# Kernel tuning notes

Hardware: AMD Instinct MI355X
Metric: run time of the kernel (lower is better)

## Reference

```python
import jax, jax.numpy as jnp
import numpy as np

D_MODEL = 1024
NHEAD = 16
HEAD_DIM = D_MODEL // NHEAD  # 64
THETA = 10000.0


def apply_rope(t):
    # t: [B, H, S, D]. Interleaved-pair RoPE (lucidrains rotary-embedding-torch
    # rotate_queries_or_keys), positions = arange(S), theta = 10000.
    B, H, S, D = t.shape
    inv_freq = 1.0 / (THETA ** (jnp.arange(0, D, 2, dtype=jnp.float32) / D))  # [D/2]
    ang = jnp.arange(S, dtype=jnp.float32)[:, None] * inv_freq               # [S, D/2]
    cos = jnp.cos(ang).astype(t.dtype)
    sin = jnp.sin(ang).astype(t.dtype)
    tp = t.reshape(B, H, S, D // 2, 2)
    x1, x2 = tp[..., 0], tp[..., 1]
    rot = jnp.stack([x1 * cos - x2 * sin, x1 * sin + x2 * cos], axis=-1)
    return rot.reshape(B, H, S, D)


def setup_inputs() -> dict:
    key = jax.random.key(0)
    k0, k1, k2, k3, k4 = jax.random.split(key, 5)
    B, Sx, Sc = 2, 2048, 2048
    sc = 0.02  # weight init scale
    return {
        "x": jax.random.normal(k0, (B, Sx, D_MODEL), jnp.float32),
        "context": jax.random.normal(k1, (B, Sc, D_MODEL), jnp.float32),
        "Wq": jax.random.normal(k2, (D_MODEL, D_MODEL), jnp.float32) * sc,
        "Wv": jax.random.normal(k3, (D_MODEL, D_MODEL), jnp.float32) * sc,
        "Wo": jax.random.normal(k4, (D_MODEL, D_MODEL), jnp.float32) * sc,
        "bo": jnp.zeros((D_MODEL,), jnp.float32),
        "x_pos": jnp.arange(B * Sx, dtype=jnp.int64).reshape(B, Sx) % Sx,
        "context_pos": jnp.arange(B * Sc, dtype=jnp.int64).reshape(B, Sc) % Sc,
    }


def reference(x, context, Wq, Wv, Wo, bo, x_pos, context_pos):
    # x_pos/context_pos are unused when both streams use the internal
    # RotaryEmbedding (is_imu1=is_imu2=True), matching the original forward.
    B, Sx, _ = x.shape
    Sc = context.shape[1]
    q = (x @ Wq.T).reshape(B, Sx, NHEAD, HEAD_DIM).transpose(0, 2, 1, 3)
    # NOTE: original code uses projq (not projk) for keys — replicated here.
    k = (context @ Wq.T).reshape(B, Sc, NHEAD, HEAD_DIM).transpose(0, 2, 1, 3)
    v = (context @ Wv.T).reshape(B, Sc, NHEAD, HEAD_DIM).transpose(0, 2, 1, 3)
    q = apply_rope(q)
    k = apply_rope(k)
    scale = 1.0 / jnp.sqrt(jnp.asarray(HEAD_DIM, q.dtype))
    attn = jax.nn.softmax(jnp.einsum("bhqd,bhkd->bhqk", q, k) * scale, axis=-1)
    out = jnp.einsum("bhqk,bhkd->bhqd", attn, v)            # [B,H,Sx,hd]
    out = out.transpose(0, 2, 1, 3).reshape(B, Sx, D_MODEL)  # [B,Sx,d_model]
    return out @ Wo.T + bo
```

## Files before the change

### kernel.cpp

```cpp
#include <hip/hip_runtime.h>
#include <cmath>


typedef __bf16 bf16x8 __attribute__((ext_vector_type(8)));
typedef __bf16 bf16x4 __attribute__((ext_vector_type(4)));
typedef float f32x4 __attribute__((ext_vector_type(4)));
typedef float f32x16 __attribute__((ext_vector_type(16)));
typedef unsigned u32x4v __attribute__((ext_vector_type(4)));

#define MFMA(A, B, C) __builtin_amdgcn_mfma_f32_16x16x32_bf16(A, B, C, 0, 0, 0)
#define MFMA32(A, B, C) __builtin_amdgcn_mfma_f32_32x32x16_bf16(A, B, C, 0, 0, 0)
#define GLL16(g, l)                                                        \
  __builtin_amdgcn_global_load_lds(                                        \
      (const __attribute__((address_space(1))) unsigned int*)(g),          \
      (__attribute__((address_space(3))) unsigned int*)(l), 16, 0, 0)

#define VMCNT(N) asm volatile("s_waitcnt vmcnt(" #N ")" ::: "memory")
#define BARM() asm volatile("s_barrier" ::: "memory")
#define LGKM0() asm volatile("s_waitcnt lgkmcnt(0)" ::: "memory")

__global__ __launch_bounds__(256) void cvt_all_kernel(
    const float* __restrict__ x, const float* __restrict__ ctx,
    const float* __restrict__ Wq, const float* __restrict__ Wv,
    const float* __restrict__ Wo, __bf16* __restrict__ xb, __bf16* __restrict__ cb,
    __bf16* __restrict__ Wqb, __bf16* __restrict__ Wvb, __bf16* __restrict__ Wob) {
  int base = blockIdx.x * 512 + threadIdx.x;
  const float* src;
  __bf16* dst;
  int off;
  if (base < 1048576) { src = x; dst = xb; off = 0; }
  else if (base < 2097152) { src = ctx; dst = cb; off = 1048576; }
  else if (base < 2359296) { src = Wq; dst = Wqb; off = 2097152; }
  else if (base < 2621440) { src = Wv; dst = Wvb; off = 2359296; }
  else { src = Wo; dst = Wob; off = 2621440; }
#pragma unroll
  for (int jj = 0; jj < 2; jj++) {
    int j = base - off + jj * 256;
    float4 f = ((const float4*)src)[j];
    bf16x4 o;
    o[0] = (__bf16)f.x; o[1] = (__bf16)f.y; o[2] = (__bf16)f.z; o[3] = (__bf16)f.w;
    ((bf16x4*)dst)[j] = o;
  }
}

__global__ __launch_bounds__(512, 2) void gemm_proj(const __bf16* __restrict__ A0,
                                                    const __bf16* __restrict__ W0,
                                                    void* __restrict__ outQ,
                                                    void* __restrict__ outK,
                                                    void* __restrict__ outV) {
  const int tid = threadIdx.x;
  const int wave = tid >> 6, lane = tid & 63, quad = lane >> 4, l15 = lane & 15;
  const int wm = wave >> 2, wn = wave & 3;

  const int id = blockIdx.x;
  int m0, n0;
  const __bf16* A;
  const __bf16* W;
  bool vmode;
  if (id < 128) {
    const int xcd = id & 7, j = id >> 3;
    m0 = (xcd * 4 + (j & 3)) * 256;
    n0 = (j >> 2) * 256;
    A = A0;
    W = W0;
    vmode = false;
  } else {
    const int vid = id - 128;
    const int xcd = vid & 7, j = vid >> 3;
    m0 = (xcd * 2 + (j & 1)) * 256;
    n0 = (j >> 1) * 256;
    A = A0 + (size_t)4096 * 1024;
    W = W0 + (size_t)1024 * 1024;
    vmode = true;
  }

  __shared__ __attribute__((aligned(16))) __bf16 As[2][2][8192];
  __shared__ __attribute__((aligned(16))) __bf16 Bs[2][2][8192];

  const int srow = tid >> 2;
  const int kcg = (tid & 3) ^ (srow & 3);
  const size_t aoff0 = (size_t)srow * 1024 + kcg * 8;
  const size_t aoff1 = (size_t)(srow + 128) * 1024 + kcg * 8;
  const __bf16* Ag = A + (size_t)m0 * 1024;
  const __bf16* Wg = W + (size_t)n0 * 1024;
  const int ldst0 = wave * 512;
  const int ldst1 = 4096 + wave * 512;

  auto stageA = [&](int slot, int kh, int kel) {
    GLL16(Ag + aoff0 + kel, &As[slot][kh][ldst0]);
    GLL16(Ag + aoff1 + kel, &As[slot][kh][ldst1]);
  };
  auto stageB = [&](int slot, int kh, int kel) {
    GLL16(Wg + aoff0 + kel, &Bs[slot][kh][ldst0]);
    GLL16(Wg + aoff1 + kel, &Bs[slot][kh][ldst1]);
  };

  const int xk = (quad ^ (l15 & 3)) * 8;
  int afo[8], bfo[4];
#pragma unroll
  for (int mf = 0; mf < 8; mf++) afo[mf] = (wm * 128 + mf * 16 + l15) * 32 + xk;
#pragma unroll
  for (int nf = 0; nf < 4; nf++) bfo[nf] = (wn * 64 + nf * 16 + l15) * 32 + xk;

  f32x4 acc[8][4] = {};
  bf16x8 bf[4], af[4];

  auto loadB = [&](int slot, int kh) {
#pragma unroll
    for (int nf = 0; nf < 4; nf++) bf[nf] = *(const bf16x8*)&Bs[slot][kh][bfo[nf]];
  };
  auto loadA = [&](int slot, int kh, int mfg) {
#pragma unroll
    for (int mf = 0; mf < 4; mf++)
      af[mf] = *(const bf16x8*)&As[slot][kh][afo[mfg * 4 + mf]];
  };
  auto mfma16 = [&](int mfg) {
    __builtin_amdgcn_s_setprio(1);
#pragma unroll
    for (int mf = 0; mf < 4; mf++)
#pragma unroll
      for (int nf = 0; nf < 4; nf++)
        acc[mfg * 4 + mf][nf] = MFMA(af[mf], bf[nf], acc[mfg * 4 + mf][nf]);
    __builtin_amdgcn_s_setprio(0);
  };

  stageA(0, 0, 0);  stageB(0, 0, 0);
  stageA(0, 1, 32); stageB(0, 1, 32);
  stageA(1, 0, 64); stageB(1, 0, 64);
  VMCNT(8); BARM();

#pragma unroll 1
  for (int j = 0; j < 7; j++) {
    const int kb = j * 128;
    loadB(0, 0); loadA(0, 0, 0); stageA(1, 1, kb + 96);
    BARM(); LGKM0(); mfma16(0); BARM();
    loadA(0, 0, 1); stageB(1, 1, kb + 96);
    BARM(); LGKM0(); mfma16(1); VMCNT(8); BARM();
    loadB(0, 1); loadA(0, 1, 0); stageA(0, 0, kb + 128);
    BARM(); LGKM0(); mfma16(0); BARM();
    loadA(0, 1, 1); stageB(0, 0, kb + 128);
    BARM(); LGKM0(); mfma16(1); VMCNT(8); BARM();
    loadB(1, 0); loadA(1, 0, 0); stageA(0, 1, kb + 160);
    BARM(); LGKM0(); mfma16(0); BARM();
    loadA(1, 0, 1); stageB(0, 1, kb + 160);
    BARM(); LGKM0(); mfma16(1); VMCNT(8); BARM();
    loadB(1, 1); loadA(1, 1, 0); stageA(1, 0, kb + 192);
    BARM(); LGKM0(); mfma16(0); BARM();
    loadA(1, 1, 1); stageB(1, 0, kb + 192);
    BARM(); LGKM0(); mfma16(1); VMCNT(8); BARM();
  }
  {
    loadB(0, 0); loadA(0, 0, 0); stageA(1, 1, 992);
    BARM(); LGKM0(); mfma16(0); BARM();
    loadA(0, 0, 1); stageB(1, 1, 992);
    BARM(); LGKM0(); mfma16(1); VMCNT(8); BARM();
    loadB(0, 1); loadA(0, 1, 0);
    BARM(); LGKM0(); mfma16(0); BARM();
    loadA(0, 1, 1);
    BARM(); LGKM0(); mfma16(1); VMCNT(4); BARM();
    loadB(1, 0); loadA(1, 0, 0);
    BARM(); LGKM0(); mfma16(0); BARM();
    loadA(1, 0, 1);
    BARM(); LGKM0(); mfma16(1); VMCNT(0); BARM();
    loadB(1, 1); loadA(1, 1, 0);
    BARM(); LGKM0(); mfma16(0); BARM();
    loadA(1, 1, 1);
    BARM(); LGKM0(); mfma16(1);
  }

  if (!vmode) {
    const int isK = (m0 >= 4096);
    __bf16* O = (__bf16*)(isK ? outK : outQ);
    const float qsc = isK ? 1.0f : 0.18033688f;
    const int mb = m0 & 4095;
#pragma unroll
    for (int nf = 0; nf < 4; nf++) {
      const int n = n0 + wn * 64 + nf * 16 + l15;
      const int h = n >> 6, d = n & 63, p = d >> 1;
      const float invf_rev =
          __builtin_amdgcn_exp2f(-((float)p * 0.41524101f + 2.6514961f));
#pragma unroll
      for (int mf = 0; mf < 8; mf++) {
#pragma unroll
        for (int r = 0; r < 4; r++) {
          const int row = mb + wm * 128 + mf * 16 + quad * 4 + r;
          const int s = row & 2047, b = row >> 11;
          float v = acc[mf][nf][r];
          float pv = __shfl_xor(v, 1, 64);
          float fr = __builtin_amdgcn_fractf((float)s * invf_rev);
          float sn = __builtin_amdgcn_sinf(fr);
          float cs = __builtin_amdgcn_cosf(fr);
          float res = (lane & 1) ? (pv * sn + v * cs) : (v * cs - pv * sn);
          O[((size_t)(b * 16 + h) * 2048 + s) * 64 + d] = (__bf16)(res * qsc);
        }
      }
    }
  } else {
    __bf16* O = (__bf16*)outV;
#pragma unroll
    for (int nf = 0; nf < 4; nf++) {
      const int n = n0 + wn * 64 + nf * 16 + l15;
      const int h = n >> 6, d = n & 63;
#pragma unroll
      for (int mf = 0; mf < 8; mf++) {
        const int rowb = m0 + wm * 128 + mf * 16 + quad * 4;
        const int s = rowb & 2047, b = rowb >> 11;
        bf16x4 o;
#pragma unroll
        for (int r = 0; r < 4; r++) o[r] = (__bf16)acc[mf][nf][r];
        *(bf16x4*)(O + ((size_t)(b * 16 + h) * 64 + d) * 2048 + s) = o;
      }
    }
  }
}

__global__ __launch_bounds__(256) void gemm_out(const __bf16* __restrict__ A,
                                                const __bf16* __restrict__ W,
                                                float* __restrict__ O,
                                                const float* __restrict__ bias) {
  const int tid = threadIdx.x;
  const int wave = tid >> 6, lane = tid & 63, quad = lane >> 4, l15 = lane & 15;
  const int mw = wave >> 1, nw = wave & 1;
  const int id = blockIdx.x;
  const int xcd = id & 7, j = id >> 3;
  const int m0 = (xcd * 4 + (j & 3)) * 128;
  const int n0 = (j >> 2) * 64;

  __shared__ __attribute__((aligned(16))) __bf16 As[3][4096];
  __shared__ __attribute__((aligned(16))) __bf16 Ws[3][2048];

  int goff[2];
#pragma unroll
  for (int jj = 0; jj < 2; jj++) {
    const int s = jj * 256 + tid;
    const int row = s >> 2;
    const int kcg = (s & 3) ^ ((row >> 1) & 3);
    goff[jj] = row * 1024 + kcg * 8;
  }
  const int wrow = tid >> 2;
  const int wkcg = (tid & 3) ^ ((wrow >> 1) & 3);
  const int goffw = wrow * 1024 + wkcg * 8;

  const __bf16* Ag = A + (size_t)m0 * 1024;
  const __bf16* Wg = W + (size_t)n0 * 1024;
  const int ldsoff0 = wave * 512;
  const int ldsoff1 = 2048 + wave * 512;

  const int sw = (l15 >> 1) & 3;
  int afoff[4], wfoff[2];
#pragma unroll
  for (int t = 0; t < 4; t++)
    afoff[t] = (mw * 64 + t * 16 + l15) * 32 + (quad ^ sw) * 8;
#pragma unroll
  for (int t = 0; t < 2; t++)
    wfoff[t] = (nw * 32 + t * 16 + l15) * 32 + (quad ^ sw) * 8;

  f32x4 acc[4][2] = {};

  auto stage = [&](int buf, int k0) {
    GLL16(Ag + goff[0] + k0, &As[buf][ldsoff0]);
    GLL16(Ag + goff[1] + k0, &As[buf][ldsoff1]);
    GLL16(Wg + goffw + k0, &Ws[buf][ldsoff0]);
  };
  auto compute = [&](int buf) {
    bf16x8 af[4], wf[2];
#pragma unroll
    for (int t = 0; t < 4; t++) af[t] = *(const bf16x8*)&As[buf][afoff[t]];
#pragma unroll
    for (int t = 0; t < 2; t++) wf[t] = *(const bf16x8*)&Ws[buf][wfoff[t]];
#pragma unroll
    for (int mt = 0; mt < 4; mt++)
#pragma unroll
      for (int nt = 0; nt < 2; nt++) acc[mt][nt] = MFMA(af[mt], wf[nt], acc[mt][nt]);
  };

  stage(0, 0);
  stage(1, 32);
  int buf = 0;
  for (int c = 0; c < 32; c++) {
    __syncthreads();
    if (c + 2 < 32) {
      int nb = buf + 2;
      if (nb >= 3) nb -= 3;
      stage(nb, (c + 2) * 32);
    }
    compute(buf);
    buf = (buf == 2) ? 0 : buf + 1;
  }

#pragma unroll
  for (int nt = 0; nt < 2; nt++) {
    const int n = n0 + nw * 32 + nt * 16 + l15;
    const float bv = bias[n];
#pragma unroll
    for (int mt = 0; mt < 4; mt++) {
#pragma unroll
      for (int r = 0; r < 4; r++) {
        const int row = m0 + mw * 64 + mt * 16 + quad * 4 + r;
        O[(size_t)row * 1024 + n] = acc[mt][nt][r] + bv;
      }
    }
  }
}

__global__ __launch_bounds__(512, 4) void attn_kernel(const __bf16* __restrict__ Q,
                                                      const __bf16* __restrict__ K,
                                                      const __bf16* __restrict__ Vt,
                                                      __bf16* __restrict__ Aout) {
  const int tid = threadIdx.x;
  const int wave = tid >> 6, lane = tid & 63;
  const int l31 = lane & 31, hi = lane >> 5;
  const int qg = wave >> 1, kg = wave & 1;
  const int id = blockIdx.x;
  const int j = id >> 3;
  const int bh = ((id & 7) << 2) | (j & 3);
  const int q0 = (j >> 2) << 7;

  const __bf16* Qb = Q + (size_t)bh * (2048 * 64);
  const __bf16* Kb = K + (size_t)bh * (2048 * 64);
  const __bf16* Vb = Vt + (size_t)bh * (64 * 2048);

  __shared__ __attribute__((aligned(16))) __bf16 Kbuf[4][4096];
  __shared__ __attribute__((aligned(16))) float Lred[512];

  bf16x8 qf[4];
  {
    const __bf16* qp = Qb + (size_t)(q0 + qg * 32 + l31) * 64 + hi * 8;
#pragma unroll
    for (int i = 0; i < 4; i++) qf[i] = *(const bf16x8*)(qp + i * 16);
  }

  const __bf16* kgp = Kb + lane * 64 + wave * 8;
  const int klds = wave * 512;

  int koff[4];
  {
    const int rk = kg * 32 + l31;
#pragma unroll
    for (int i = 0; i < 4; i++) koff[i] = (2 * i + hi) * 512 + rk * 8;
  }
  const __bf16* vgb = Vb + (size_t)l31 * 2048 + (kg * 4 + hi) * 8;

  f32x4 rs4 = {};
  f32x16 oacc[2] = {};

  auto stageK = [&](int buf, int kt) { GLL16(kgp + kt * 64, &Kbuf[buf][klds]); };

  auto loadV = [&](bf16x8 (&vf)[2][2], int ktb) {
#pragma unroll
    for (int dt = 0; dt < 2; dt++)
#pragma unroll
      for (int ks = 0; ks < 2; ks++)
        vf[dt][ks] = *(const bf16x8*)(vgb + (size_t)dt * 32 * 2048 + ktb + ks * 16);
  };

  auto compute = [&](int buf, const bf16x8 (&vf)[2][2]) {
    f32x16 s = {};
#pragma unroll
    for (int i = 0; i < 4; i++) {
      bf16x8 kf = *(const bf16x8*)&Kbuf[buf][koff[i]];
      s = MFMA32(kf, qf[i], s);
    }
    float pe[16];
#pragma unroll
    for (int r = 0; r < 16; r++) pe[r] = __builtin_amdgcn_exp2f(s[r]);
#pragma unroll
    for (int r = 0; r < 16; r++) rs4[r & 3] += pe[r];
    bf16x8 pa[2];
#pragma unroll
    for (int sl = 0; sl < 2; sl++) {
      unsigned wa, wb, wc, wd;
      asm("v_cvt_pk_bf16_f32 %0, %1, %2" : "=v"(wa) : "v"(pe[8 * sl + 0]), "v"(pe[8 * sl + 1]));
      asm("v_cvt_pk_bf16_f32 %0, %1, %2" : "=v"(wb) : "v"(pe[8 * sl + 4]), "v"(pe[8 * sl + 5]));
      asm("v_cvt_pk_bf16_f32 %0, %1, %2" : "=v"(wc) : "v"(pe[8 * sl + 2]), "v"(pe[8 * sl + 3]));
      asm("v_cvt_pk_bf16_f32 %0, %1, %2" : "=v"(wd) : "v"(pe[8 * sl + 6]), "v"(pe[8 * sl + 7]));
      asm("v_permlane32_swap_b32 %0, %1" : "+v"(wa), "+v"(wb));
      asm("v_permlane32_swap_b32 %0, %1" : "+v"(wc), "+v"(wd));
      u32x4v t;
      t[0] = wa; t[1] = wc; t[2] = wb; t[3] = wd;
      pa[sl] = __builtin_bit_cast(bf16x8, t);
    }
#pragma unroll
    for (int dt = 0; dt < 2; dt++)
#pragma unroll
      for (int ks = 0; ks < 2; ks++)
        oacc[dt] = MFMA32(pa[ks], vf[dt][ks], oacc[dt]);
  };

  bf16x8 vX[2][2], vY[2][2];
  loadV(vX, 0);
  stageK(0, 0);
  stageK(1, 64);
  for (int kt = 0; kt < 2048; kt += 128) {
    const int p = (kt >> 7) & 1;
    __syncthreads();
    if (kt + 128 < 2048) {
      stageK(2 * (p ^ 1), kt + 128);
      stageK(2 * (p ^ 1) + 1, kt + 192);
    }
    loadV(vY, kt + 64);
    compute(2 * p, vX);
    if (kt + 128 < 2048) loadV(vX, kt + 128);
    compute(2 * p + 1, vY);
  }

  __syncthreads();
  float* Ored = (float*)&Kbuf[0][0];

  float lw = (rs4[0] + rs4[1]) + (rs4[2] + rs4[3]);
  lw += __shfl_xor(lw, 32, 64);
  Lred[wave * 64 + lane] = lw;
  if (kg == 1) {
#pragma unroll
    for (int dt = 0; dt < 2; dt++)
#pragma unroll
      for (int r = 0; r < 16; r++)
        Ored[(qg * 32 + dt * 16 + r) * 64 + lane] = oacc[dt][r];
  }
  __syncthreads();
  if (kg == 0) {
    const int b = bh >> 4, h = bh & 15;
#pragma unroll
    for (int r = 0; r < 16; r++) {
      const int qrow = (r & 3) + 8 * (r >> 2) + 4 * hi;
      const float lt =
          Lred[(qg * 2) * 64 + qrow] + Lred[(qg * 2 + 1) * 64 + qrow];
      const float inv = 1.f / lt;
      const int qAbs = q0 + qg * 32 + qrow;
#pragma unroll
      for (int dt = 0; dt < 2; dt++) {
        const float o = oacc[dt][r] + Ored[(qg * 32 + dt * 16 + r) * 64 + lane];
        Aout[((size_t)(b * 2048 + qAbs)) * 1024 + h * 64 + dt * 32 + l31] =
            (__bf16)(o * inv);
      }
    }
  }
}

extern "C" void kernel_launch(void* const* d_in, const int* in_sizes, int n_in,
                              void* d_out, int out_size, void* d_ws, size_t ws_size,
                              hipStream_t stream) {
  const float* x   = (const float*)d_in[0];
  const float* ctx = (const float*)d_in[1];
  const float* Wq  = (const float*)d_in[2];
  const float* Wv  = (const float*)d_in[3];
  const float* Wo  = (const float*)d_in[4];
  const float* bo  = (const float*)d_in[5];

  char* ws = (char*)d_ws;
  const size_t MB = 1024 * 1024;
  __bf16* xb   = (__bf16*)(ws + 0 * MB);
  __bf16* cb   = (__bf16*)(ws + 8 * MB);
  __bf16* Wqb  = (__bf16*)(ws + 16 * MB);
  __bf16* Wvb  = (__bf16*)(ws + 18 * MB);
  __bf16* Wob  = (__bf16*)(ws + 20 * MB);
  __bf16* qh   = (__bf16*)(ws + 22 * MB);
  __bf16* kh   = (__bf16*)(ws + 30 * MB);
  __bf16* vt   = (__bf16*)(ws + 38 * MB);
  __bf16* attn = xb;

  cvt_all_kernel<<<5632, 256, 0, stream>>>(x, ctx, Wq, Wv, Wo, xb, cb, Wqb, Wvb, Wob);

  gemm_proj<<<192, 512, 0, stream>>>(xb, Wqb, (void*)qh, (void*)kh, (void*)vt);

  attn_kernel<<<512, 512, 0, stream>>>(qh, kh, vt, attn);

  gemm_out<<<512, 256, 0, stream>>>(attn, Wob, (float*)d_out, bo);
}
```

Measured before the change: 233.3 us.

## Pre-swizzle K and V into MFMA fragment layout and drop LDS staging in attention

The projection epilogue now writes K and V in a tiled layout that matches the MFMA fragment order. This lets the attention kernel load K fragments straight from global memory into registers with contiguous 16-byte loads, instead of staging them through LDS with global_load_lds and per-tile barriers. The main loop becomes barrier-free, double-buffered register prefetch of K and V. Launch bounds drop from 4 to 2 blocks per CU to give more registers for the extra buffers. The cost is more global/L2 traffic per wave, since each wave loads its K fragments independently, and possibly lower occupancy.

```diff
diff --git a/kernel.cpp b/kernel.cpp
--- a/kernel.cpp
+++ b/kernel.cpp
@@ -173,25 +173,52 @@
     __bf16* O = (__bf16*)(isK ? outK : outQ);
     const float qsc = isK ? 1.0f : 0.18033688f;
     const int mb = m0 & 4095;
-#pragma unroll
-    for (int nf = 0; nf < 4; nf++) {
-      const int n = n0 + wn * 64 + nf * 16 + l15;
-      const int h = n >> 6, d = n & 63, p = d >> 1;
-      const float invf_rev =
-          __builtin_amdgcn_exp2f(-((float)p * 0.41524101f + 2.6514961f));
-#pragma unroll
-      for (int mf = 0; mf < 8; mf++) {
-#pragma unroll
-        for (int r = 0; r < 4; r++) {
-          const int row = mb + wm * 128 + mf * 16 + quad * 4 + r;
-          const int s = row & 2047, b = row >> 11;
-          float v = acc[mf][nf][r];
-          float pv = __shfl_xor(v, 1, 64);
-          float fr = __builtin_amdgcn_fractf((float)s * invf_rev);
-          float sn = __builtin_amdgcn_sinf(fr);
-          float cs = __builtin_amdgcn_cosf(fr);
-          float res = (lane & 1) ? (pv * sn + v * cs) : (v * cs - pv * sn);
-          O[((size_t)(b * 16 + h) * 2048 + s) * 64 + d] = (__bf16)(res * qsc);
+    if (!isK) {
+#pragma unroll
+      for (int nf = 0; nf < 4; nf++) {
+        const int n = n0 + wn * 64 + nf * 16 + l15;
+        const int h = n >> 6, d = n & 63, p = d >> 1;
+        const float invf_rev =
+            __builtin_amdgcn_exp2f(-((float)p * 0.41524101f + 2.6514961f));
+#pragma unroll
+        for (int mf = 0; mf < 8; mf++) {
+#pragma unroll
+          for (int r = 0; r < 4; r++) {
+            const int row = mb + wm * 128 + mf * 16 + quad * 4 + r;
+            const int s = row & 2047, b = row >> 11;
+            float v = acc[mf][nf][r];
+            float pv = __shfl_xor(v, 1, 64);
+            float fr = __builtin_amdgcn_fractf((float)s * invf_rev);
+            float sn = __builtin_amdgcn_sinf(fr);
+            float cs = __builtin_amdgcn_cosf(fr);
+            float res = (lane & 1) ? (pv * sn + v * cs) : (v * cs - pv * sn);
+            O[((size_t)(b * 16 + h) * 2048 + s) * 64 + d] = (__bf16)(res * qsc);
+          }
+        }
+      }
+    } else {
+#pragma unroll
+      for (int nf = 0; nf < 4; nf++) {
+        const int n = n0 + wn * 64 + nf * 16 + l15;
+        const int h = n >> 6, d = n & 63, p = d >> 1;
+        const float invf_rev =
+            __builtin_amdgcn_exp2f(-((float)p * 0.41524101f + 2.6514961f));
+#pragma unroll
+        for (int mf = 0; mf < 8; mf++) {
+#pragma unroll
+          for (int r = 0; r < 4; r++) {
+            const int row = mb + wm * 128 + mf * 16 + quad * 4 + r;
+            const int s = row & 2047, b = row >> 11;
+            float v = acc[mf][nf][r];
+            float pv = __shfl_xor(v, 1, 64);
+            float fr = __builtin_amdgcn_fractf((float)s * invf_rev);
+            float sn = __builtin_amdgcn_sinf(fr);
+            float cs = __builtin_amdgcn_cosf(fr);
+            float res = (lane & 1) ? (pv * sn + v * cs) : (v * cs - pv * sn);
+            O[(size_t)(b * 16 + h) * 131072 +
+              (size_t)((s >> 5) * 8 + (d >> 3)) * 256 + (s & 31) * 8 + (d & 7)] =
+                (__bf16)res;
+          }
         }
       }
     }
@@ -208,7 +235,8 @@
         bf16x4 o;
 #pragma unroll
         for (int r = 0; r < 4; r++) o[r] = (__bf16)acc[mf][nf][r];
-        *(bf16x4*)(O + ((size_t)(b * 16 + h) * 64 + d) * 2048 + s) = o;
+        *(bf16x4*)(O + (size_t)(b * 16 + h) * 131072 + (size_t)(s >> 3) * 512 +
+                   d * 8 + (s & 7)) = o;
       }
     }
   }
@@ -303,7 +331,7 @@
   }
 }
 
-__global__ __launch_bounds__(512, 4) void attn_kernel(const __bf16* __restrict__ Q,
+__global__ __launch_bounds__(512, 2) void attn_kernel(const __bf16* __restrict__ Q,
                                                       const __bf16* __restrict__ K,
                                                       const __bf16* __restrict__ Vt,
                                                       __bf16* __restrict__ Aout) {
@@ -317,11 +345,11 @@
   const int q0 = (j >> 2) << 7;
 
   const __bf16* Qb = Q + (size_t)bh * (2048 * 64);
-  const __bf16* Kb = K + (size_t)bh * (2048 * 64);
-  const __bf16* Vb = Vt + (size_t)bh * (64 * 2048);
-
-  __shared__ __attribute__((aligned(16))) __bf16 Kbuf[4][4096];
-  __shared__ __attribute__((aligned(16))) float Lred[512];
+  const __bf16* Kp = K + (size_t)bh * 131072;
+  const __bf16* Vp = Vt + (size_t)bh * 131072;
+
+  __shared__ float Ored[4][32][64];
+  __shared__ float Lred[512];
 
   bf16x8 qf[4];
   {
@@ -330,37 +358,30 @@
     for (int i = 0; i < 4; i++) qf[i] = *(const bf16x8*)(qp + i * 16);
   }
 
-  const __bf16* kgp = Kb + lane * 64 + wave * 8;
-  const int klds = wave * 512;
-
-  int koff[4];
-  {
-    const int rk = kg * 32 + l31;
-#pragma unroll
-    for (int i = 0; i < 4; i++) koff[i] = (2 * i + hi) * 512 + rk * 8;
-  }
-  const __bf16* vgb = Vb + (size_t)l31 * 2048 + (kg * 4 + hi) * 8;
+  const __bf16* kfr = Kp + kg * 2048 + hi * 256 + l31 * 8;
+  const __bf16* vfr = Vp + (kg * 4 + hi) * 512 + l31 * 8;
 
   f32x4 rs4 = {};
   f32x16 oacc[2] = {};
 
-  auto stageK = [&](int buf, int kt) { GLL16(kgp + kt * 64, &Kbuf[buf][klds]); };
-
-  auto loadV = [&](bf16x8 (&vf)[2][2], int ktb) {
+  auto loadK = [&](bf16x8 (&kf)[4], int kt) {
+#pragma unroll
+    for (int i = 0; i < 4; i++)
+      kf[i] = *(const bf16x8*)(kfr + (size_t)kt * 64 + i * 512);
+  };
+  auto loadV = [&](bf16x8 (&vf)[2][2], int kt) {
 #pragma unroll
     for (int dt = 0; dt < 2; dt++)
 #pragma unroll
       for (int ks = 0; ks < 2; ks++)
-        vf[dt][ks] = *(const bf16x8*)(vgb + (size_t)dt * 32 * 2048 + ktb + ks * 16);
-  };
-
-  auto compute = [&](int buf, const bf16x8 (&vf)[2][2]) {
+        vf[dt][ks] =
+            *(const bf16x8*)(vfr + (size_t)kt * 64 + ks * 1024 + dt * 256);
+  };
+
+  auto compute = [&](const bf16x8 (&kf)[4], const bf16x8 (&vf)[2][2]) {
     f32x16 s = {};
 #pragma unroll
-    for (int i = 0; i < 4; i++) {
-      bf16x8 kf = *(const bf16x8*)&Kbuf[buf][koff[i]];
-      s = MFMA32(kf, qf[i], s);
-    }
+    for (int i = 0; i < 4; i++) s = MFMA32(kf[i], qf[i], s);
     float pe[16];
 #pragma unroll
     for (int r = 0; r < 16; r++) pe[r] = __builtin_amdgcn_exp2f(s[r]);
@@ -387,25 +408,20 @@
         oacc[dt] = MFMA32(pa[ks], vf[dt][ks], oacc[dt]);
   };
 
-  bf16x8 vX[2][2], vY[2][2];
-  loadV(vX, 0);
-  stageK(0, 0);
-  stageK(1, 64);
+  bf16x8 kfA[4], vfA[2][2], kfB[4], vfB[2][2];
+  loadK(kfA, 0);
+  loadV(vfA, 0);
+#pragma unroll 1
   for (int kt = 0; kt < 2048; kt += 128) {
-    const int p = (kt >> 7) & 1;
-    __syncthreads();
+    loadK(kfB, kt + 64);
+    loadV(vfB, kt + 64);
+    compute(kfA, vfA);
     if (kt + 128 < 2048) {
-      stageK(2 * (p ^ 1), kt + 128);
-      stageK(2 * (p ^ 1) + 1, kt + 192);
-    }
-    loadV(vY, kt + 64);
-    compute(2 * p, vX);
-    if (kt + 128 < 2048) loadV(vX, kt + 128);
-    compute(2 * p + 1, vY);
-  }
-
-  __syncthreads();
-  float* Ored = (float*)&Kbuf[0][0];
+      loadK(kfA, kt + 128);
+      loadV(vfA, kt + 128);
+    }
+    compute(kfB, vfB);
+  }
 
   float lw = (rs4[0] + rs4[1]) + (rs4[2] + rs4[3]);
   lw += __shfl_xor(lw, 32, 64);
@@ -415,7 +431,7 @@
     for (int dt = 0; dt < 2; dt++)
 #pragma unroll
       for (int r = 0; r < 16; r++)
-        Ored[(qg * 32 + dt * 16 + r) * 64 + lane] = oacc[dt][r];
+        Ored[qg][dt * 16 + r][lane] = oacc[dt][r];
   }
   __syncthreads();
   if (kg == 0) {
@@ -429,7 +445,7 @@
       const int qAbs = q0 + qg * 32 + qrow;
 #pragma unroll
       for (int dt = 0; dt < 2; dt++) {
-        const float o = oacc[dt][r] + Ored[(qg * 32 + dt * 16 + r) * 64 + lane];
+        const float o = oacc[dt][r] + Ored[qg][dt * 16 + r][lane];
         Aout[((size_t)(b * 2048 + qAbs)) * 1024 + h * 64 + dt * 32 + l31] =
             (__bf16)(o * inv);
       }
```

Result: faster. 200.2 us (-14.2%).
